# Kernel optimization log

Hardware: AMD Instinct MI355X
Metric: run time of the kernel (lower is better)

## Reference

```python
import jax, jax.numpy as jnp
from jax import lax
import numpy as np

B, L, C_CH, HH, WW = 2, 5, 64, 100, 352
DOWNSAMPLE_RATE = 2
DISCRETE_RATIO = 0.4  # voxel_size[0]
KEEP_FRAC = 4  # keep top H*W//4 locations per non-ego agent


def setup_inputs() -> dict:
    key = jax.random.key(0)
    k1, k2, k3, k4 = jax.random.split(key, 4)
    N = B * L
    x = jax.random.normal(k1, (N, C_CH, HH, WW), jnp.float32)
    psm = jax.random.normal(k2, (N, 2, HH, WW), jnp.float32)
    record_len = jnp.full((B,), L, dtype=jnp.int32)
    # homogeneous transforms: identity + small perturbation so warps stay mostly in-bounds
    eye = jnp.eye(4, dtype=jnp.float32)
    pairwise_t_matrix = eye + 0.05 * jax.random.normal(k3, (B, L, L, 4, 4), jnp.float32)
    fuse_w = 0.02 * jax.random.normal(k4, (C_CH, C_CH, 7, 7), jnp.float32)
    fuse_b = jnp.zeros((C_CH,), jnp.float32)
    return {"x": x, "psm": psm, "record_len": record_len,
            "pairwise_t_matrix": pairwise_t_matrix, "fuse_w": fuse_w, "fuse_b": fuse_b}


def _bilinear_sample(img, px, py):
    # img [C,H,W]; px,py pixel coords [H,W]; zero padding (grid_sample padding_mode='zeros')
    C, H, W = img.shape
    x0 = jnp.floor(px); y0 = jnp.floor(py)
    wx1 = px - x0; wx0 = 1.0 - wx1
    wy1 = py - y0; wy0 = 1.0 - wy1

    def gather(yy, xx):
        yi = jnp.clip(yy, 0, H - 1).astype(jnp.int32)
        xi = jnp.clip(xx, 0, W - 1).astype(jnp.int32)
        val = img[:, yi, xi]  # [C,H,W]
        valid = ((yy >= 0) & (yy <= H - 1) & (xx >= 0) & (xx <= W - 1)).astype(img.dtype)
        return val * valid

    return (gather(y0, x0) * (wy0 * wx0) + gather(y0, x0 + 1) * (wy0 * wx1)
            + gather(y0 + 1, x0) * (wy1 * wx0) + gather(y0 + 1, x0 + 1) * (wy1 * wx1))


def _affine_warp(img, theta):
    # warp_affine_simple: F.affine_grid + F.grid_sample, align_corners=False
    C, H, W = img.shape
    ys = (jnp.arange(H, dtype=img.dtype) + 0.5) * (2.0 / H) - 1.0
    xs = (jnp.arange(W, dtype=img.dtype) + 0.5) * (2.0 / W) - 1.0
    gy, gx = jnp.meshgrid(ys, xs, indexing='ij')  # [H,W]
    src_x = theta[0, 0] * gx + theta[0, 1] * gy + theta[0, 2]
    src_y = theta[1, 0] * gx + theta[1, 1] * gy + theta[1, 2]
    px = (src_x + 1.0) * (W * 0.5) - 0.5
    py = (src_y + 1.0) * (H * 0.5) - 0.5
    return _bilinear_sample(img, px, py)


def _forward(x, psm, pairwise_t_matrix, fuse_w, fuse_b):
    N, C, H, W = x.shape
    Bp, Lp = pairwise_t_matrix.shape[:2]
    # take 2x3 affine part: rows [0,1], cols [0,1,3]
    t = pairwise_t_matrix[..., :2, :][..., jnp.array([0, 1, 3])]  # [B,L,L,2,3]
    scale = jnp.array([[1.0, H / W, 2.0 / (DOWNSAMPLE_RATE * DISCRETE_RATIO * W)],
                       [W / H, 1.0, 2.0 / (DOWNSAMPLE_RATE * DISCRETE_RATIO * H)]], dtype=x.dtype)
    t = t * scale
    # ego row (t_matrix[0, :N]): warp every agent into the ego frame
    thetas = t[:, 0].reshape(N, 2, 3)  # [N,2,3]

    # Communication: confidence map = sigmoid(max over anchor channels)
    conf = jax.nn.sigmoid(jnp.max(psm, axis=1, keepdims=True))  # [N,1,H,W]

    warp = jax.vmap(_affine_warp)
    x_w = warp(x, thetas)          # [N,C,H,W]
    conf_w = warp(conf, thetas)    # [N,1,H,W]

    # confidence-driven sparsification: keep top H*W//KEEP_FRAC locations per agent
    K = (H * W) // KEEP_FRAC
    flat = conf_w.reshape(N, H * W)
    kth = lax.top_k(flat, K)[0][:, -1]                      # [N]
    mask = (flat >= kth[:, None]).astype(x.dtype).reshape(N, 1, H, W)
    is_ego = (jnp.arange(N) % Lp) == 0                      # ego keeps everything
    mask = jnp.where(is_ego[:, None, None, None], jnp.ones_like(mask), mask)

    sparse = x_w * mask
    fused = lax.conv_general_dilated(sparse, fuse_w, (1, 1), [(3, 3), (3, 3)],
                                     dimension_numbers=('NCHW', 'OIHW', 'NCHW'))
    fused = fused + fuse_b[None, :, None, None]
    # per-scene fusion across agents (mean aggregation)
    out = fused.reshape(Bp, Lp, C, H, W).mean(axis=1)  # [B,C,H,W]
    return out


def reference(x, psm, record_len, pairwise_t_matrix, fuse_w, fuse_b):
    del record_len  # regular case: every scene has L agents
    return _forward(x, psm, pairwise_t_matrix, fuse_w, fuse_b)
```

## Files before the change

kernel.cpp:

```cpp
#include <hip/hip_runtime.h>
#include <hip/hip_bf16.h>

#define HH 100
#define WW 352
#define NB 2
#define LL 5
#define NN 10
#define CCH 64
#define HW (HH*WW)
#define KTOP (HW/4)
#define HP (HH+6)
#define WP 390

typedef __bf16 bf16x8 __attribute__((ext_vector_type(8)));
typedef float f32x4 __attribute__((ext_vector_type(4)));

#define WS_CONF  0u
#define WS_TAU   1408000u
#define WS_WTP   1408064u
#define WS_PAD   1809472u
#define WS_XT    12392512u
#define PAD_BYTES ((size_t)NB*HP*WP*CCH*2)


__device__ __forceinline__ void load_theta(const float* __restrict__ ptm, int b, int l, float th[6]) {
#pragma clang fp contract(off)
  const float* tb = ptm + ((b*LL + 0)*LL + l)*16;
  th[0] = tb[0] * 1.0f;
  th[1] = tb[1] * (float)(100.0/352.0);
  th[2] = tb[3] * (float)(2.0/(2.0*0.4*352.0));
  th[3] = tb[4] * (float)(352.0/100.0);
  th[4] = tb[5] * 1.0f;
  th[5] = tb[7] * (float)(2.0/(2.0*0.4*100.0));
}

__global__ void conf_warp_kernel(const float* __restrict__ psm,
                                 const float* __restrict__ ptm,
                                 float* __restrict__ conf_w) {
#pragma clang fp contract(off)
  int w = blockIdx.x * 128 + threadIdx.x;
  int h = blockIdx.y;
  int n = blockIdx.z;
  if (w >= WW) return;
  int b = n / LL, l = n % LL;
  float th[6];
  load_theta(ptm, b, l, th);
  float gy = ((float)h + 0.5f) * (float)(2.0/100.0) - 1.0f;
  float gx = ((float)w + 0.5f) * (float)(2.0/352.0) - 1.0f;
  float sx = th[0]*gx + th[1]*gy + th[2];
  float sy = th[3]*gx + th[4]*gy + th[5];
  float px = (sx + 1.0f) * ((float)WW * 0.5f) - 0.5f;
  float py = (sy + 1.0f) * ((float)HH * 0.5f) - 0.5f;
  float x0 = floorf(px), y0 = floorf(py);
  float wx1 = px - x0, wx0 = 1.0f - wx1;
  float wy1 = py - y0, wy0 = 1.0f - wy1;
  const float* p0 = psm + (size_t)(n*2 + 0)*HW;
  const float* p1 = psm + (size_t)(n*2 + 1)*HW;
  float yy[2] = {y0, y0 + 1.0f};
  float xx[2] = {x0, x0 + 1.0f};
  float wgt[2][2] = {{wy0*wx0, wy0*wx1}, {wy1*wx0, wy1*wx1}};
  float out = 0.0f;
  for (int iy = 0; iy < 2; ++iy) {
    for (int ix = 0; ix < 2; ++ix) {
      float yv = yy[iy], xv = xx[ix];
      float yc = fminf(fmaxf(yv, 0.0f), (float)(HH-1));
      float xc = fminf(fmaxf(xv, 0.0f), (float)(WW-1));
      int yi = (int)yc, xi = (int)xc;
      int idx = yi*WW + xi;
      float m = fmaxf(p0[idx], p1[idx]);
      float v = 1.0f / (1.0f + expf(-m));
      bool valid = (yv >= 0.0f) && (yv <= (float)(HH-1)) && (xv >= 0.0f) && (xv <= (float)(WW-1));
      out += (valid ? v : 0.0f) * wgt[iy][ix];
    }
  }
  conf_w[(size_t)n*HW + h*WW + w] = out;
}

__device__ __forceinline__ unsigned int scan_incl(unsigned int v, int lane, int wid,
                                                  volatile unsigned int* wsum) {
  unsigned int inc = v;
  for (int off = 1; off < 64; off <<= 1) {
    unsigned int o = __shfl_up(inc, off);
    if (lane >= off) inc += o;
  }
  if (lane == 63) wsum[wid] = inc;
  __syncthreads();
  unsigned int wadd = 0;
  for (int w2 = 0; w2 < wid; ++w2) wadd += wsum[w2];
  return inc + wadd;
}

__global__ __launch_bounds__(256) void topk_kernel(const float* __restrict__ conf_w,
                                                   float* __restrict__ tau) {
  __shared__ unsigned int hist[16384];
  __shared__ unsigned int wsum[4];
  __shared__ unsigned int s_pref, s_mask, s_k;
  int n = blockIdx.x;
  int tid = threadIdx.x, lane = tid & 63, wid = tid >> 6;
  const float4* src = (const float4*)(conf_w + (size_t)n*HW);
  if (tid == 0) { s_pref = 0u; s_mask = 0u; s_k = KTOP; }
  __syncthreads();
  const int shifts[3] = {18, 4, 0};
  const int widths[3] = {14, 14, 4};
  for (int r = 0; r < 3; ++r) {
    int shift = shifts[r];
    int nbins = 1 << widths[r];
    unsigned int fmask = (unsigned int)(nbins - 1);
    for (int i = tid; i < nbins; i += 256) hist[i] = 0u;
    __syncthreads();
    unsigned int maskhi = s_mask, pref = s_pref, k = s_k;
    for (int i = tid; i < HW/4; i += 256) {
      float4 v = src[i];
      unsigned int u0 = __float_as_uint(v.x);
      unsigned int u1 = __float_as_uint(v.y);
      unsigned int u2 = __float_as_uint(v.z);
      unsigned int u3 = __float_as_uint(v.w);
      if ((u0 & maskhi) == pref) atomicAdd(&hist[(u0 >> shift) & fmask], 1u);
      if ((u1 & maskhi) == pref) atomicAdd(&hist[(u1 >> shift) & fmask], 1u);
      if ((u2 & maskhi) == pref) atomicAdd(&hist[(u2 >> shift) & fmask], 1u);
      if ((u3 & maskhi) == pref) atomicAdd(&hist[(u3 >> shift) & fmask], 1u);
    }
    __syncthreads();
    int C = nbins >> 8; if (C == 0) C = 1;
    int active = (C * 256 > nbins) ? nbins : 256;
    int top = nbins - 1 - tid*C;
    unsigned int csum = 0u;
    if (tid < active)
      for (int i = 0; i < C; ++i) csum += hist[top - i];
    unsigned int incl = scan_incl(csum, lane, wid, wsum);
    unsigned int excl = incl - csum;
    if (tid < active && excl < k && incl >= k) {
      unsigned int run = excl;
      for (int i = 0; i < C; ++i) {
        unsigned int c = hist[top - i];
        if (run + c >= k) {
          unsigned int bin = (unsigned int)(top - i);
          s_pref = pref | (bin << shift);
          s_mask = maskhi | (fmask << shift);
          s_k = k - run;
          break;
        }
        run += c;
      }
    }
    __syncthreads();
  }
  if (tid == 0) tau[n] = __uint_as_float(s_pref);
}

__global__ void pack_w_kernel(const float* __restrict__ fw, __bf16* __restrict__ wtp) {
  int idx = blockIdx.x*256 + threadIdx.x;
  if (idx >= CCH*CCH*49) return;
  int c = idx & 63;
  int k = (idx >> 6) & 63;
  int dydx = idx >> 12;
  wtp[((size_t)dydx*CCH + k)*CCH + c] = (__bf16)fw[((size_t)k*CCH + c)*49 + dydx];
}

__global__ __launch_bounds__(256) void repack_x_kernel(const float* __restrict__ x,
                                                       __bf16* __restrict__ xT) {
  __shared__ float tile[64][65];
  int n = blockIdx.y;
  int px0 = blockIdx.x * 64;
  int tid = threadIdx.x;
  int pxl = tid & 63;
  int c0 = tid >> 6;
  const float* xs = x + (size_t)n*CCH*HW + px0 + pxl;
#pragma unroll
  for (int i = 0; i < 16; ++i) {
    int c = c0 + i*4;
    tile[c][pxl] = xs[(size_t)c*HW];
  }
  __syncthreads();
  int px2 = tid >> 2;
  int cc0 = (tid & 3) * 16;
  __bf16 vv[16];
#pragma unroll
  for (int j = 0; j < 16; ++j) vv[j] = (__bf16)tile[cc0 + j][px2];
  __bf16* dst = xT + ((size_t)n*HW + px0 + px2)*CCH + cc0;
  *reinterpret_cast<bf16x8*>(dst)     = *reinterpret_cast<bf16x8*>(&vv[0]);
  *reinterpret_cast<bf16x8*>(dst + 8) = *reinterpret_cast<bf16x8*>(&vv[8]);
}

__global__ __launch_bounds__(256) void warp_avg_kernel(
    const __bf16* __restrict__ xT, const float* __restrict__ ptm,
    const float* __restrict__ conf_w, const float* __restrict__ tau,
    __bf16* __restrict__ pad) {
  int idx = blockIdx.x*256 + threadIdx.x;
  int px = idx >> 2;
  int ch0 = (idx & 3) * 16;
  int b = (px >= HW) ? 1 : 0;
  int rem = px - b*HW;
  int h = rem / WW;
  int w = rem - h*WW;
  float acc[16];
#pragma unroll
  for (int i = 0; i < 16; ++i) acc[i] = 0.0f;
  float gy = ((float)h + 0.5f) * (float)(2.0/100.0) - 1.0f;
  float gx = ((float)w + 0.5f) * (float)(2.0/352.0) - 1.0f;
  for (int l = 0; l < LL; ++l) {
    int n = b*LL + l;
    if (l != 0 && !(conf_w[(size_t)n*HW + rem] >= tau[n])) continue;
    float th[6];
    load_theta(ptm, b, l, th);
    float sx = th[0]*gx + th[1]*gy + th[2];
    float sy = th[3]*gx + th[4]*gy + th[5];
    float fpx = (sx + 1.0f) * ((float)WW*0.5f) - 0.5f;
    float fpy = (sy + 1.0f) * ((float)HH*0.5f) - 0.5f;
    float x0 = floorf(fpx), y0 = floorf(fpy);
    float wx1 = fpx - x0, wx0 = 1.0f - wx1;
    float wy1 = fpy - y0, wy0 = 1.0f - wy1;
    float y1 = y0 + 1.0f, x1 = x0 + 1.0f;
    bool vy0 = (y0 >= 0.0f) && (y0 <= (float)(HH-1));
    bool vy1 = (y1 >= 0.0f) && (y1 <= (float)(HH-1));
    bool vx0 = (x0 >= 0.0f) && (x0 <= (float)(WW-1));
    bool vx1 = (x1 >= 0.0f) && (x1 <= (float)(WW-1));
    int yi0 = (int)fminf(fmaxf(y0, 0.0f), (float)(HH-1));
    int yi1 = (int)fminf(fmaxf(y1, 0.0f), (float)(HH-1));
    int xi0 = (int)fminf(fmaxf(x0, 0.0f), (float)(WW-1));
    int xi1 = (int)fminf(fmaxf(x1, 0.0f), (float)(WW-1));
    float wgt[4] = { wy0*wx0 * ((vy0 && vx0) ? 1.0f : 0.0f),
                     wy0*wx1 * ((vy0 && vx1) ? 1.0f : 0.0f),
                     wy1*wx0 * ((vy1 && vx0) ? 1.0f : 0.0f),
                     wy1*wx1 * ((vy1 && vx1) ? 1.0f : 0.0f) };
    int off[4] = { yi0*WW + xi0, yi0*WW + xi1, yi1*WW + xi0, yi1*WW + xi1 };
#pragma unroll
    for (int t4 = 0; t4 < 4; ++t4) {
      if (wgt[t4] == 0.0f) continue;
      float wt = wgt[t4];
      const __bf16* src = xT + ((size_t)n*HW + off[t4])*CCH + ch0;
#pragma unroll
      for (int ch = 0; ch < 2; ++ch) {
        bf16x8 v = *reinterpret_cast<const bf16x8*>(src + ch*8);
#pragma unroll
        for (int e = 0; e < 8; ++e) acc[ch*8 + e] += wt * (float)v[e];
      }
    }
  }
  char* rowb = (char*)pad + (size_t)((b*HP + (h+3))*WP)*128;
  int px_p = w + 3;
  int key = (px_p & 7) << 4;
#pragma unroll
  for (int ch = 0; ch < 2; ++ch) {
    bf16x8 o;
#pragma unroll
    for (int e = 0; e < 8; ++e) o[e] = (__bf16)(acc[ch*8 + e]*0.2f);
    int slotb = (ch0*2 + ch*16) ^ key;
    *reinterpret_cast<bf16x8*>(rowb + (size_t)px_p*128 + slotb) = o;
  }
}


#define AFREAD(DX) do { \
  _Pragma("unroll") for (int m = 0; m < 2; ++m) { \
    af[m][0] = *(const bf16x8*)&wlds[((DX)*32 + m*16 + l16)*64 + cj0*8]; \
    af[m][1] = *(const bf16x8*)&wlds[((DX)*32 + m*16 + l16)*64 + cj1*8]; } } while(0)

__global__ __launch_bounds__(256, 2) void conv_kernel(
    const __bf16* __restrict__ pad, const __bf16* __restrict__ wtp,
    const float* __restrict__ fb, float* __restrict__ out) {
  __shared__ __bf16 wlds[7*32*64];
  __shared__ __bf16 plds[4][4608];
  int tid = threadIdx.x;
  int wave = tid >> 6, lane = tid & 63;
  int quad = lane >> 4, l16 = lane & 15;
  int r8 = lane >> 3, jc = lane & 7;
  int jcr = (jc - r8) & 7;
  int cj0 = (quad + l16) & 7;
  int cj1 = (quad + 4 + l16) & 7;
  int bz = blockIdx.z;
  int b = bz >> 1, kh = bz & 1;
  int h0 = blockIdx.y*4;
  int h = h0 + wave;
  int w0 = blockIdx.x*64;

  f32x4 acc[2][4];
#pragma unroll
  for (int m = 0; m < 2; ++m)
#pragma unroll
    for (int n = 0; n < 4; ++n) acc[m][n] = (f32x4){0.f,0.f,0.f,0.f};

  bf16x8 af[2][2];

#pragma unroll 1
  for (int dy = 0; dy < 7; ++dy) {
    __syncthreads();
    const __bf16* wdy = wtp + dy*28672;
#pragma unroll
    for (int j = 0; j < 7; ++j) {
      int q = wave*7 + j;
      int srcrow = (q >> 2)*64 + kh*32 + (q & 3)*8 + r8;
      __builtin_amdgcn_global_load_lds(
          (const __attribute__((address_space(1))) void*)(wdy + srcrow*64 + jcr*8),
          (__attribute__((address_space(3))) void*)&wlds[q*512], 16, 0, 0);
    }
    const __bf16* prow_g = pad + (size_t)((b*HP + h + dy)*WP + w0)*CCH;
#pragma unroll
    for (int j = 0; j < 9; ++j) {
      __builtin_amdgcn_global_load_lds(
          (const __attribute__((address_space(1))) void*)(prow_g + j*512 + lane*8),
          (__attribute__((address_space(3))) void*)&plds[wave][j*512], 16, 0, 0);
    }
    __syncthreads();
#pragma unroll
    for (int dx = 0; dx < 7; ++dx) {
      AFREAD(dx);
      bf16x8 bf[4][2];
#pragma unroll
      for (int n = 0; n < 4; ++n) {
        int p = dx + n*16 + l16;
        int key = (p & 7) << 4;
#pragma unroll
        for (int kc = 0; kc < 2; ++kc) {
          int slotb = ((quad + 4*kc) << 4) ^ key;
          bf[n][kc] = *(const bf16x8*)((const char*)&plds[wave][0] + p*128 + slotb);
        }
      }
#pragma unroll
      for (int kc = 0; kc < 2; ++kc)
#pragma unroll
        for (int m = 0; m < 2; ++m)
#pragma unroll
          for (int n = 0; n < 4; ++n)
            acc[m][n] = __builtin_amdgcn_mfma_f32_16x16x32_bf16(af[m][kc], bf[n][kc], acc[m][n], 0, 0, 0);
    }
  }

#pragma unroll
  for (int n = 0; n < 4; ++n) {
    int wpix = w0 + n*16 + l16;
    if (wpix < WW) {
#pragma unroll
      for (int m = 0; m < 2; ++m) {
#pragma unroll
        for (int rr = 0; rr < 4; ++rr) {
          int kg = kh*32 + m*16 + quad*4 + rr;
          out[((size_t)(b*CCH + kg)*HH + h)*WW + wpix] = acc[m][n][rr] + fb[kg];
        }
      }
    }
  }
}

extern "C" void kernel_launch(void* const* d_in, const int* in_sizes, int n_in,
                              void* d_out, int out_size, void* d_ws, size_t ws_size,
                              hipStream_t stream) {
  (void)in_sizes; (void)n_in; (void)out_size; (void)ws_size;
  const float* x   = (const float*)d_in[0];
  const float* psm = (const float*)d_in[1];
  const float* ptm = (const float*)d_in[3];
  const float* fw  = (const float*)d_in[4];
  const float* fb  = (const float*)d_in[5];
  float* out = (float*)d_out;
  char* ws = (char*)d_ws;
  float*  conf = (float*)(ws + WS_CONF);
  float*  tau  = (float*)(ws + WS_TAU);
  __bf16* wtp  = (__bf16*)(ws + WS_WTP);
  __bf16* pad  = (__bf16*)(ws + WS_PAD);
  __bf16* xT   = (__bf16*)(ws + WS_XT);

  hipMemsetAsync(pad, 0, PAD_BYTES, stream);
  conf_warp_kernel<<<dim3(3, HH, NN), 128, 0, stream>>>(psm, ptm, conf);
  pack_w_kernel<<<(CCH*CCH*49 + 255)/256, 256, 0, stream>>>(fw, wtp);
  repack_x_kernel<<<dim3(HW/64, NN), 256, 0, stream>>>(x, xT);
  topk_kernel<<<NN, 256, 0, stream>>>(conf, tau);
  warp_avg_kernel<<<dim3(NB*HW*4/256), 256, 0, stream>>>(xT, ptm, conf, tau, pad);
  conv_kernel<<<dim3(6, 25, NB*2), 256, 0, stream>>>(pad, wtp, fb, out);
}
```

Before: 263.3 us.

## Fuse first top-k histogram pass into confidence warp and cache thetas in LDS

```diff
diff --git a/kernel.cpp b/kernel.cpp
--- a/kernel.cpp
+++ b/kernel.cpp
@@ -20,6 +20,7 @@
 #define WS_WTP   1408064u
 #define WS_PAD   1809472u
 #define WS_XT    12392512u
+#define WS_GH    57448512u
 #define PAD_BYTES ((size_t)NB*HP*WP*CCH*2)
 
 
@@ -34,46 +35,60 @@
   th[5] = tb[7] * (float)(2.0/(2.0*0.4*100.0));
 }
 
-__global__ void conf_warp_kernel(const float* __restrict__ psm,
-                                 const float* __restrict__ ptm,
-                                 float* __restrict__ conf_w) {
+__global__ __launch_bounds__(256) void conf_topk1_kernel(const float* __restrict__ psm,
+                                                         const float* __restrict__ ptm,
+                                                         float* __restrict__ conf_w,
+                                                         unsigned int* __restrict__ gh) {
 #pragma clang fp contract(off)
-  int w = blockIdx.x * 128 + threadIdx.x;
-  int h = blockIdx.y;
-  int n = blockIdx.z;
-  if (w >= WW) return;
+  __shared__ unsigned int hist[16384];
+  int s = blockIdx.x;
+  int n = blockIdx.y;
+  int tid = threadIdx.x;
+  for (int i = tid; i < 16384; i += 256) hist[i] = 0u;
   int b = n / LL, l = n % LL;
   float th[6];
   load_theta(ptm, b, l, th);
-  float gy = ((float)h + 0.5f) * (float)(2.0/100.0) - 1.0f;
-  float gx = ((float)w + 0.5f) * (float)(2.0/352.0) - 1.0f;
-  float sx = th[0]*gx + th[1]*gy + th[2];
-  float sy = th[3]*gx + th[4]*gy + th[5];
-  float px = (sx + 1.0f) * ((float)WW * 0.5f) - 0.5f;
-  float py = (sy + 1.0f) * ((float)HH * 0.5f) - 0.5f;
-  float x0 = floorf(px), y0 = floorf(py);
-  float wx1 = px - x0, wx0 = 1.0f - wx1;
-  float wy1 = py - y0, wy0 = 1.0f - wy1;
   const float* p0 = psm + (size_t)(n*2 + 0)*HW;
   const float* p1 = psm + (size_t)(n*2 + 1)*HW;
-  float yy[2] = {y0, y0 + 1.0f};
-  float xx[2] = {x0, x0 + 1.0f};
-  float wgt[2][2] = {{wy0*wx0, wy0*wx1}, {wy1*wx0, wy1*wx1}};
-  float out = 0.0f;
-  for (int iy = 0; iy < 2; ++iy) {
-    for (int ix = 0; ix < 2; ++ix) {
-      float yv = yy[iy], xv = xx[ix];
-      float yc = fminf(fmaxf(yv, 0.0f), (float)(HH-1));
-      float xc = fminf(fmaxf(xv, 0.0f), (float)(WW-1));
-      int yi = (int)yc, xi = (int)xc;
-      int idx = yi*WW + xi;
-      float m = fmaxf(p0[idx], p1[idx]);
-      float v = 1.0f / (1.0f + expf(-m));
-      bool valid = (yv >= 0.0f) && (yv <= (float)(HH-1)) && (xv >= 0.0f) && (xv <= (float)(WW-1));
-      out += (valid ? v : 0.0f) * wgt[iy][ix];
-    }
-  }
-  conf_w[(size_t)n*HW + h*WW + w] = out;
+  __syncthreads();
+  int i0 = s * (HW/8);
+  for (int i = i0 + tid; i < i0 + HW/8; i += 256) {
+    int h = i / WW, w = i - h*WW;
+    float gy = ((float)h + 0.5f) * (float)(2.0/100.0) - 1.0f;
+    float gx = ((float)w + 0.5f) * (float)(2.0/352.0) - 1.0f;
+    float sx = th[0]*gx + th[1]*gy + th[2];
+    float sy = th[3]*gx + th[4]*gy + th[5];
+    float px = (sx + 1.0f) * ((float)WW * 0.5f) - 0.5f;
+    float py = (sy + 1.0f) * ((float)HH * 0.5f) - 0.5f;
+    float x0 = floorf(px), y0 = floorf(py);
+    float wx1 = px - x0, wx0 = 1.0f - wx1;
+    float wy1 = py - y0, wy0 = 1.0f - wy1;
+    float yy[2] = {y0, y0 + 1.0f};
+    float xx[2] = {x0, x0 + 1.0f};
+    float wgt[2][2] = {{wy0*wx0, wy0*wx1}, {wy1*wx0, wy1*wx1}};
+    float out = 0.0f;
+    for (int iy = 0; iy < 2; ++iy) {
+      for (int ix = 0; ix < 2; ++ix) {
+        float yv = yy[iy], xv = xx[ix];
+        float yc = fminf(fmaxf(yv, 0.0f), (float)(HH-1));
+        float xc = fminf(fmaxf(xv, 0.0f), (float)(WW-1));
+        int yi = (int)yc, xi = (int)xc;
+        int idx = yi*WW + xi;
+        float m = fmaxf(p0[idx], p1[idx]);
+        float v = 1.0f / (1.0f + expf(-m));
+        bool valid = (yv >= 0.0f) && (yv <= (float)(HH-1)) && (xv >= 0.0f) && (xv <= (float)(WW-1));
+        out += (valid ? v : 0.0f) * wgt[iy][ix];
+      }
+    }
+    conf_w[(size_t)n*HW + i] = out;
+    unsigned int u = __float_as_uint(out);
+    atomicAdd(&hist[(u >> 18) & 16383u], 1u);
+  }
+  __syncthreads();
+  for (int i = tid; i < 16384; i += 256) {
+    unsigned int c = hist[i];
+    if (c) atomicAdd(&gh[n*16384 + i], c);
+  }
 }
 
 __device__ __forceinline__ unsigned int scan_incl(unsigned int v, int lane, int wid,
@@ -91,6 +106,7 @@
 }
 
 __global__ __launch_bounds__(256) void topk_kernel(const float* __restrict__ conf_w,
+                                                   const unsigned int* __restrict__ gh,
                                                    float* __restrict__ tau) {
   __shared__ unsigned int hist[16384];
   __shared__ unsigned int wsum[4];
@@ -106,21 +122,27 @@
     int shift = shifts[r];
     int nbins = 1 << widths[r];
     unsigned int fmask = (unsigned int)(nbins - 1);
-    for (int i = tid; i < nbins; i += 256) hist[i] = 0u;
-    __syncthreads();
-    unsigned int maskhi = s_mask, pref = s_pref, k = s_k;
-    for (int i = tid; i < HW/4; i += 256) {
-      float4 v = src[i];
-      unsigned int u0 = __float_as_uint(v.x);
-      unsigned int u1 = __float_as_uint(v.y);
-      unsigned int u2 = __float_as_uint(v.z);
-      unsigned int u3 = __float_as_uint(v.w);
-      if ((u0 & maskhi) == pref) atomicAdd(&hist[(u0 >> shift) & fmask], 1u);
-      if ((u1 & maskhi) == pref) atomicAdd(&hist[(u1 >> shift) & fmask], 1u);
-      if ((u2 & maskhi) == pref) atomicAdd(&hist[(u2 >> shift) & fmask], 1u);
-      if ((u3 & maskhi) == pref) atomicAdd(&hist[(u3 >> shift) & fmask], 1u);
-    }
-    __syncthreads();
+    if (r == 0) {
+      for (int i = tid; i < 16384; i += 256) hist[i] = gh[n*16384 + i];
+      __syncthreads();
+    } else {
+      for (int i = tid; i < nbins; i += 256) hist[i] = 0u;
+      __syncthreads();
+      unsigned int maskhi = s_mask, pref = s_pref;
+      for (int i = tid; i < HW/4; i += 256) {
+        float4 v = src[i];
+        unsigned int u0 = __float_as_uint(v.x);
+        unsigned int u1 = __float_as_uint(v.y);
+        unsigned int u2 = __float_as_uint(v.z);
+        unsigned int u3 = __float_as_uint(v.w);
+        if ((u0 & maskhi) == pref) atomicAdd(&hist[(u0 >> shift) & fmask], 1u);
+        if ((u1 & maskhi) == pref) atomicAdd(&hist[(u1 >> shift) & fmask], 1u);
+        if ((u2 & maskhi) == pref) atomicAdd(&hist[(u2 >> shift) & fmask], 1u);
+        if ((u3 & maskhi) == pref) atomicAdd(&hist[(u3 >> shift) & fmask], 1u);
+      }
+      __syncthreads();
+    }
+    unsigned int k = s_k;
     int C = nbins >> 8; if (C == 0) C = 1;
     int active = (C * 256 > nbins) ? nbins : 256;
     int top = nbins - 1 - tid*C;
@@ -135,8 +157,8 @@
         unsigned int c = hist[top - i];
         if (run + c >= k) {
           unsigned int bin = (unsigned int)(top - i);
-          s_pref = pref | (bin << shift);
-          s_mask = maskhi | (fmask << shift);
+          s_pref = s_pref | (bin << shift);
+          s_mask = s_mask | (fmask << shift);
           s_k = k - run;
           break;
         }
@@ -186,7 +208,26 @@
     const __bf16* __restrict__ xT, const float* __restrict__ ptm,
     const float* __restrict__ conf_w, const float* __restrict__ tau,
     __bf16* __restrict__ pad) {
-  int idx = blockIdx.x*256 + threadIdx.x;
+  __shared__ float sth[NN][6];
+  __shared__ float stau[NN];
+  int tid = threadIdx.x;
+  if (tid < NN*6) {
+    int bl = tid / 6, j = tid - bl*6;
+    int bb = bl / LL, ll = bl - bb*LL;
+    const float* tb = ptm + ((bb*LL + 0)*LL + ll)*16;
+    float v;
+    if      (j == 0) v = tb[0] * 1.0f;
+    else if (j == 1) v = tb[1] * (float)(100.0/352.0);
+    else if (j == 2) v = tb[3] * (float)(2.0/(2.0*0.4*352.0));
+    else if (j == 3) v = tb[4] * (float)(352.0/100.0);
+    else if (j == 4) v = tb[5] * 1.0f;
+    else             v = tb[7] * (float)(2.0/(2.0*0.4*100.0));
+    sth[bl][j] = v;
+  }
+  if (tid >= 64 && tid < 64 + NN) stau[tid - 64] = tau[tid - 64];
+  __syncthreads();
+
+  int idx = blockIdx.x*256 + tid;
   int px = idx >> 2;
   int ch0 = (idx & 3) * 16;
   int b = (px >= HW) ? 1 : 0;
@@ -200,11 +241,9 @@
   float gx = ((float)w + 0.5f) * (float)(2.0/352.0) - 1.0f;
   for (int l = 0; l < LL; ++l) {
     int n = b*LL + l;
-    if (l != 0 && !(conf_w[(size_t)n*HW + rem] >= tau[n])) continue;
-    float th[6];
-    load_theta(ptm, b, l, th);
-    float sx = th[0]*gx + th[1]*gy + th[2];
-    float sy = th[3]*gx + th[4]*gy + th[5];
+    if (l != 0 && !(conf_w[(size_t)n*HW + rem] >= stau[n])) continue;
+    float sx = sth[n][0]*gx + sth[n][1]*gy + sth[n][2];
+    float sy = sth[n][3]*gx + sth[n][4]*gy + sth[n][5];
     float fpx = (sx + 1.0f) * ((float)WW*0.5f) - 0.5f;
     float fpy = (sy + 1.0f) * ((float)HH*0.5f) - 0.5f;
     float x0 = floorf(fpx), y0 = floorf(fpy);
@@ -358,12 +397,14 @@
   __bf16* wtp  = (__bf16*)(ws + WS_WTP);
   __bf16* pad  = (__bf16*)(ws + WS_PAD);
   __bf16* xT   = (__bf16*)(ws + WS_XT);
+  unsigned int* gh = (unsigned int*)(ws + WS_GH);
 
   hipMemsetAsync(pad, 0, PAD_BYTES, stream);
-  conf_warp_kernel<<<dim3(3, HH, NN), 128, 0, stream>>>(psm, ptm, conf);
+  hipMemsetAsync(gh, 0, (size_t)NN*16384*4, stream);
   pack_w_kernel<<<(CCH*CCH*49 + 255)/256, 256, 0, stream>>>(fw, wtp);
   repack_x_kernel<<<dim3(HW/64, NN), 256, 0, stream>>>(x, xT);
-  topk_kernel<<<NN, 256, 0, stream>>>(conf, tau);
+  conf_topk1_kernel<<<dim3(8, NN), 256, 0, stream>>>(psm, ptm, conf, gh);
+  topk_kernel<<<NN, 256, 0, stream>>>(conf, gh, tau);
   warp_avg_kernel<<<dim3(NB*HW*4/256), 256, 0, stream>>>(xT, ptm, conf, tau, pad);
   conv_kernel<<<dim3(6, 25, NB*2), 256, 0, stream>>>(pad, wtp, fb, out);
 }
```

After: 290.3 us. +10.2%, slower.

## Double-buffer conv LDS staging to overlap next-row loads with MFMA

Applied to the files above, without the earlier changes.

```diff
diff --git a/kernel.cpp b/kernel.cpp
--- a/kernel.cpp
+++ b/kernel.cpp
@@ -251,16 +251,33 @@
 }
 
 
-#define AFREAD(DX) do { \
+#define STAGE(BUF, DY) do { \
+  const __bf16* wdy_ = wtp + (DY)*28672; \
+  _Pragma("unroll") for (int j = 0; j < 7; ++j) { \
+    int q = wave*7 + j; \
+    int srcrow = (q >> 2)*64 + kh*32 + (q & 3)*8 + r8; \
+    __builtin_amdgcn_global_load_lds( \
+        (const __attribute__((address_space(1))) void*)(wdy_ + srcrow*64 + jcr*8), \
+        (__attribute__((address_space(3))) void*)&wlds[BUF][q*512], 16, 0, 0); \
+  } \
+  const __bf16* prow_ = pad + (size_t)((b*HP + h + (DY))*WP + w0)*CCH; \
+  _Pragma("unroll") for (int j = 0; j < 9; ++j) { \
+    __builtin_amdgcn_global_load_lds( \
+        (const __attribute__((address_space(1))) void*)(prow_ + j*512 + lane*8), \
+        (__attribute__((address_space(3))) void*)&plds[BUF][wave][j*512], 16, 0, 0); \
+  } \
+} while (0)
+
+#define AFREAD(BUF, DX) do { \
   _Pragma("unroll") for (int m = 0; m < 2; ++m) { \
-    af[m][0] = *(const bf16x8*)&wlds[((DX)*32 + m*16 + l16)*64 + cj0*8]; \
-    af[m][1] = *(const bf16x8*)&wlds[((DX)*32 + m*16 + l16)*64 + cj1*8]; } } while(0)
-
-__global__ __launch_bounds__(256, 2) void conv_kernel(
+    af[m][0] = *(const bf16x8*)&wlds[BUF][((DX)*32 + m*16 + l16)*64 + cj0*8]; \
+    af[m][1] = *(const bf16x8*)&wlds[BUF][((DX)*32 + m*16 + l16)*64 + cj1*8]; } } while (0)
+
+__global__ __launch_bounds__(256, 1) void conv_kernel(
     const __bf16* __restrict__ pad, const __bf16* __restrict__ wtp,
     const float* __restrict__ fb, float* __restrict__ out) {
-  __shared__ __bf16 wlds[7*32*64];
-  __shared__ __bf16 plds[4][4608];
+  __shared__ __bf16 wlds[2][7*32*64];
+  __shared__ __bf16 plds[2][4][4608];
   int tid = threadIdx.x;
   int wave = tid >> 6, lane = tid & 63;
   int quad = lane >> 4, l16 = lane & 15;
@@ -282,29 +299,16 @@
 
   bf16x8 af[2][2];
 
+  STAGE(0, 0);
+  __syncthreads();
+
 #pragma unroll 1
   for (int dy = 0; dy < 7; ++dy) {
-    __syncthreads();
-    const __bf16* wdy = wtp + dy*28672;
-#pragma unroll
-    for (int j = 0; j < 7; ++j) {
-      int q = wave*7 + j;
-      int srcrow = (q >> 2)*64 + kh*32 + (q & 3)*8 + r8;
-      __builtin_amdgcn_global_load_lds(
-          (const __attribute__((address_space(1))) void*)(wdy + srcrow*64 + jcr*8),
-          (__attribute__((address_space(3))) void*)&wlds[q*512], 16, 0, 0);
-    }
-    const __bf16* prow_g = pad + (size_t)((b*HP + h + dy)*WP + w0)*CCH;
-#pragma unroll
-    for (int j = 0; j < 9; ++j) {
-      __builtin_amdgcn_global_load_lds(
-          (const __attribute__((address_space(1))) void*)(prow_g + j*512 + lane*8),
-          (__attribute__((address_space(3))) void*)&plds[wave][j*512], 16, 0, 0);
-    }
-    __syncthreads();
+    int cur = dy & 1;
+    if (dy < 6) STAGE(cur ^ 1, dy + 1);
 #pragma unroll
     for (int dx = 0; dx < 7; ++dx) {
-      AFREAD(dx);
+      AFREAD(cur, dx);
       bf16x8 bf[4][2];
 #pragma unroll
       for (int n = 0; n < 4; ++n) {
@@ -313,7 +317,7 @@
 #pragma unroll
         for (int kc = 0; kc < 2; ++kc) {
           int slotb = ((quad + 4*kc) << 4) ^ key;
-          bf[n][kc] = *(const bf16x8*)((const char*)&plds[wave][0] + p*128 + slotb);
+          bf[n][kc] = *(const bf16x8*)((const char*)&plds[cur][wave][0] + p*128 + slotb);
         }
       }
 #pragma unroll
@@ -324,6 +328,7 @@
           for (int n = 0; n < 4; ++n)
             acc[m][n] = __builtin_amdgcn_mfma_f32_16x16x32_bf16(af[m][kc], bf[n][kc], acc[m][n], 0, 0, 0);
     }
+    __syncthreads();
   }
 
 #pragma unroll
```

After: 278.5 us. +5.8%, slower.
